# Kernel tuning notes

Measured on AMD Instinct MI355X. Metric: run time of the kernel, lower is better.

## Reference

```python
import jax, jax.numpy as jnp
import numpy as np

B, N, H = 32, 1024, 512
THR = 0.05  # peak_detection_threshold


def _l2norm(x):
    return x / jnp.linalg.norm(x, axis=-1, keepdims=True)


def setup_inputs() -> dict:
    key = jax.random.key(0)
    ks = jax.random.split(key, 6)
    def w(k, shape, fan_in):
        return jax.random.normal(k, shape, jnp.float32) / np.float32(np.sqrt(fan_in))
    return {
        "segment_rep": jax.random.normal(ks[0], (B, N, H), jnp.float32),
        "phn_mask": jnp.ones((B, N), jnp.float32),
        # SegmentSimilarityMeasure: Linear(2H->H), ReLU, Linear(H->1, no bias)
        "W1": w(ks[1], (2 * H, H), 2 * H),
        "b1": jnp.zeros((H,), jnp.float32),
        "W2": w(ks[2], (H, 1), H),
        # word_enc: Linear(H->H), ReLU, Linear(H->H)
        "We1": w(ks[3], (H, H), H),
        "be1": jnp.zeros((H,), jnp.float32),
        "We2": w(ks[4], (H, H), H),
        "be2": jnp.zeros((H,), jnp.float32),
    }


def _forward(segment_rep, phn_mask, W1, b1, W2, We1, be1, We2, be2):
    Bs, Np, Hd = segment_rep.shape
    # adjacent segment similarity: MLP on concat of l2-normalized neighbors -> (B, N-1)
    cat = jnp.concatenate([_l2norm(segment_rep[:, :-1, :]), _l2norm(segment_rep[:, 1:, :])], axis=2)
    S = (jax.nn.relu(cat @ W1 + b1) @ W2)[..., 0]

    # relative dissimilarity
    Smin = jnp.min(S, axis=1, keepdims=True)
    Smax = jnp.max(S, axis=1, keepdims=True)
    D = 1.0 - (S - Smin) / (Smax - Smin)

    # peak detector (faithful to original, incl. final overwrite of first-order cols -2:)
    z = jnp.zeros_like(D)
    fo = z
    fo = fo.at[:, 0].set(jnp.maximum(D[:, 0] - D[:, 1], 0.0))
    fo = fo.at[:, 1:-1].set(jnp.minimum(jnp.maximum(D[:, 1:-1] - D[:, :-2], 0.0),
                                        jnp.maximum(D[:, 1:-1] - D[:, 2:], 0.0)))
    fo = fo.at[:, -1].set(jnp.maximum(D[:, -1] - D[:, -2], 0.0))
    so = z
    so = so.at[:, 0:2].set(jnp.maximum(D[:, 0:2] - D[:, 2:4], 0.0))
    so = so.at[:, 2:-2].set(jnp.minimum(jnp.maximum(D[:, 2:-2] - D[:, :-4], 0.0),
                                        jnp.maximum(D[:, 2:-2] - D[:, 4:], 0.0)))
    fo = fo.at[:, -2:].set(jnp.maximum(D[:, -2:] - D[:, -4:-2], 0.0))  # replicates original code
    P = jnp.minimum(jnp.maximum(jnp.maximum(fo, so) - THR, 0.0), fo)

    # pad, mask, straight-through hard boundaries
    P = jnp.pad(P, ((0, 0), (0, 1)))
    P = jax.nn.relu(P + (phn_mask - 1.0))
    b_soft = jnp.tanh(10.0 * P)
    b_hard = jnp.tanh(100000.0 * P)
    b = b_soft + jax.lax.stop_gradient(b_hard - b_soft)
    b = jnp.cumsum(b, axis=1)  # (B, N)
    b = b + (b[:, :1] == 0).astype(b.dtype)  # per-row +1 if b[:,0]==0
    num_word_segments = b[:, -1].astype(jnp.int32) + 1  # (B,)

    # U: column j holds j+1 for j < num_word_segments[i], else -100000. Nmax = N (static bound).
    cols = jnp.arange(1, Np + 1, dtype=jnp.int32)  # (Nmax,)
    U = jnp.where(cols[None, :] <= num_word_segments[:, None],
                  cols.astype(segment_rep.dtype)[None, :], -100000.0)  # (B, Nmax)

    V = U[:, None, :] - b[:, :, None]  # (B, N, Nmax)
    Wseg = 1.0 - jnp.tanh(100000.0 * jnp.abs(V))
    Wseg = Wseg / jnp.sum(Wseg, axis=1, keepdims=True)
    Wseg = jnp.nan_to_num(Wseg)

    # pool: (B, Nmax, N) @ (B, N, H) -> (B, Nmax, H)
    word_rep = jnp.einsum('bnm,bnh->bmh', Wseg, segment_rep)
    word_masks = jnp.where(word_rep == 0, 0.0, 1.0)
    out = jax.nn.relu(word_rep @ We1 + be1) @ We2 + be2
    return out * word_masks


def reference(segment_rep, phn_mask, W1, b1, W2, We1, be1, We2, be2):
    return _forward(segment_rep, phn_mask, W1, b1, W2, We1, be1, We2, be2)
```

## Files before the change

### kernel.cpp

```cpp
#include <hip/hip_runtime.h>

#define BB 32
#define NN 1024
#define HH 512
#define NS 1023

typedef unsigned short u16;
typedef unsigned int   u32;
typedef __attribute__((ext_vector_type(8))) short bf16x8;
typedef __attribute__((ext_vector_type(4))) float f32x4;

__device__ __forceinline__ float bf2f(u16 h) {
  union { u32 u; float f; } c; c.u = ((u32)h) << 16; return c.f;
}
__device__ __forceinline__ u16 f2bf(float f) {
  union { float f; u32 u; } c; c.f = f;
  u32 u = c.u;
  return (u16)((u + 0x7fffu + ((u >> 16) & 1u)) >> 16);
}
__device__ __forceinline__ void split_bf(float x, u16& hi, u16& lo) {
  hi = f2bf(x);
  lo = f2bf(x - bf2f(hi));
}
__device__ __forceinline__ void dma16(const u16* g, u16* l) {
  __builtin_amdgcn_global_load_lds(
      (const __attribute__((address_space(1))) u32*)g,
      (__attribute__((address_space(3))) u32*)l, 16, 0, 0);
}

__global__ __launch_bounds__(64) void k_prep_a(const float* __restrict__ seg,
                                               u16* __restrict__ ahi,
                                               u16* __restrict__ alo) {
  int row = blockIdx.x, lane = threadIdx.x;
  const float4* p = (const float4*)(seg + ((size_t)row << 9) + lane * 8);
  float4 a = p[0], b = p[1];
  float v[8] = {a.x, a.y, a.z, a.w, b.x, b.y, b.z, b.w};
  float s = 0.f;
#pragma unroll
  for (int i = 0; i < 8; ++i) s += v[i] * v[i];
#pragma unroll
  for (int m = 32; m; m >>= 1) s += __shfl_xor(s, m, 64);
  float nrm = sqrtf(s);
  u16 h[8], l[8];
#pragma unroll
  for (int i = 0; i < 8; ++i) split_bf(v[i] / nrm, h[i], l[i]);
  size_t off = ((size_t)row << 9) + lane * 8;
  *(uint4*)(ahi + off) = make_uint4(h[0] | (h[1] << 16), h[2] | (h[3] << 16),
                                    h[4] | (h[5] << 16), h[6] | (h[7] << 16));
  *(uint4*)(alo + off) = make_uint4(l[0] | (l[1] << 16), l[2] | (l[3] << 16),
                                    l[4] | (l[5] << 16), l[6] | (l[7] << 16));
}

__global__ __launch_bounds__(256) void k_tr(const float* __restrict__ src,
                                            u16* __restrict__ dh,
                                            u16* __restrict__ dl,
                                            int K, int N) {
  __shared__ u16 Th[64 * 66], Tl[64 * 66];
  int nb = blockIdx.x * 64, kb = blockIdx.y * 64;
  int tid = threadIdx.x;
#pragma unroll
  for (int i = 0; i < 16; ++i) {
    int e = tid + i * 256;
    int r = e >> 6, c = e & 63;
    float v = src[(size_t)(kb + r) * N + nb + c];
    u16 hi, lo; split_bf(v, hi, lo);
    Th[c * 66 + r] = hi;
    Tl[c * 66 + r] = lo;
  }
  __syncthreads();
#pragma unroll
  for (int i = 0; i < 16; ++i) {
    int e = tid + i * 256;
    int n = e >> 6, k = e & 63;
    dh[(size_t)(nb + n) * K + kb + k] = Th[n * 66 + k];
    if (dl) dl[(size_t)(nb + n) * K + kb + k] = Tl[n * 66 + k];
  }
}

__global__ __launch_bounds__(512, 2) void k_sgemm(const u16* __restrict__ ahi,
                                                  const u16* __restrict__ alo,
                                                  const u16* __restrict__ w1h,
                                                  const u16* __restrict__ w1l,
                                                  const float* __restrict__ b1,
                                                  const float* __restrict__ W2,
                                                  float* __restrict__ Spart) {
  __shared__ u16 Ah[2][256 * 32];
  __shared__ u16 Al[2][256 * 32];
  __shared__ u16 Bh[2][256 * 32];
  __shared__ u16 Bl[2][256 * 32];

  const int tid  = threadIdx.x;
  const int wave = tid >> 6, lane = tid & 63;
  const int quad = lane >> 4, l15 = lane & 15;
  const int wm = wave >> 2, wn = wave & 3;
  const int r_in = lane >> 2, c_in = lane & 3;
  const int nblk = blockIdx.x, mblk = blockIdx.y;
  const int mrow0 = mblk * 256;
  const int ncol0 = nblk * 256;

#define SG_AH(tb_, ks_)                                                      \
  {                                                                          \
    int k0_ = (ks_) * 32, half_ = k0_ >> 9, cb_ = k0_ & 511;                 \
    int g0_ = mrow0 + wave * 32 + r_in + half_;                              \
    int g1_ = g0_ + 16;                                                      \
    if (g0_ > 32767) g0_ = 32767;                                            \
    if (g1_ > 32767) g1_ = 32767;                                            \
    dma16(ahi + ((((size_t)g0_) << 9) + cb_ + c_in * 8),                     \
          &Ah[tb_][(wave * 32) * 32]);                                       \
    dma16(ahi + ((((size_t)g1_) << 9) + cb_ + c_in * 8),                     \
          &Ah[tb_][(wave * 32 + 16) * 32]);                                  \
  }
#define SG_AL(tb_, ks_)                                                      \
  {                                                                          \
    int k0_ = (ks_) * 32, half_ = k0_ >> 9, cb_ = k0_ & 511;                 \
    int g0_ = mrow0 + wave * 32 + r_in + half_;                              \
    int g1_ = g0_ + 16;                                                      \
    if (g0_ > 32767) g0_ = 32767;                                            \
    if (g1_ > 32767) g1_ = 32767;                                            \
    dma16(alo + ((((size_t)g0_) << 9) + cb_ + c_in * 8),                     \
          &Al[tb_][(wave * 32) * 32]);                                       \
    dma16(alo + ((((size_t)g1_) << 9) + cb_ + c_in * 8),                     \
          &Al[tb_][(wave * 32 + 16) * 32]);                                  \
  }
#define SG_BH(tb_, ks_)                                                      \
  {                                                                          \
    int k0_ = (ks_) * 32;                                                    \
    int n0_ = ncol0 + wave * 32 + r_in;                                      \
    dma16(w1h + (((size_t)n0_) << 10) + k0_ + c_in * 8,                      \
          &Bh[tb_][(wave * 32) * 32]);                                       \
    dma16(w1h + (((size_t)(n0_ + 16)) << 10) + k0_ + c_in * 8,               \
          &Bh[tb_][(wave * 32 + 16) * 32]);                                  \
  }
#define SG_BL(tb_, ks_)                                                      \
  {                                                                          \
    int k0_ = (ks_) * 32;                                                    \
    int n0_ = ncol0 + wave * 32 + r_in;                                      \
    dma16(w1l + (((size_t)n0_) << 10) + k0_ + c_in * 8,                      \
          &Bl[tb_][(wave * 32) * 32]);                                       \
    dma16(w1l + (((size_t)(n0_ + 16)) << 10) + k0_ + c_in * 8,               \
          &Bl[tb_][(wave * 32 + 16) * 32]);                                  \
  }

  f32x4 acc[8][4];
#pragma unroll
  for (int mi = 0; mi < 8; ++mi)
#pragma unroll
    for (int ni = 0; ni < 4; ++ni) acc[mi][ni] = (f32x4){0.f, 0.f, 0.f, 0.f};

  SG_AH(0, 0) SG_BH(0, 0) SG_BL(0, 0) SG_AL(0, 0)
  asm volatile("s_waitcnt vmcnt(4)" ::: "memory");
  __builtin_amdgcn_s_barrier();

  for (int ks = 0; ks < 32; ++ks) {
    const int bb = ks & 1;
    const int nx = (ks + 1 < 32) ? ks + 1 : 31;
    bf16x8 ah[8], al[8], bh[4], bl[4];

#pragma unroll
    for (int mi = 0; mi < 8; ++mi)
      ah[mi] = *(const bf16x8*)&Ah[bb][(wm * 128 + mi * 16 + l15) * 32 + quad * 8];
#pragma unroll
    for (int ni = 0; ni < 4; ++ni)
      bh[ni] = *(const bf16x8*)&Bh[bb][(wn * 64 + ni * 16 + l15) * 32 + quad * 8];
    SG_AH(bb ^ 1, nx) SG_BH(bb ^ 1, nx)
    asm volatile("s_waitcnt lgkmcnt(0)" ::: "memory");
    __builtin_amdgcn_sched_barrier(0);
    __builtin_amdgcn_s_setprio(1);
#pragma unroll
    for (int ni = 0; ni < 4; ++ni)
#pragma unroll
      for (int mi = 0; mi < 8; ++mi)
        acc[mi][ni] = __builtin_amdgcn_mfma_f32_16x16x32_bf16(ah[mi], bh[ni], acc[mi][ni], 0, 0, 0);
    __builtin_amdgcn_s_setprio(0);
    asm volatile("s_waitcnt vmcnt(6)" ::: "memory");
    __builtin_amdgcn_s_barrier();

#pragma unroll
    for (int ni = 0; ni < 4; ++ni)
      bl[ni] = *(const bf16x8*)&Bl[bb][(wn * 64 + ni * 16 + l15) * 32 + quad * 8];
    SG_BL(bb ^ 1, nx) SG_AL(bb ^ 1, nx)
    asm volatile("s_waitcnt lgkmcnt(0)" ::: "memory");
    __builtin_amdgcn_sched_barrier(0);
    __builtin_amdgcn_s_setprio(1);
#pragma unroll
    for (int ni = 0; ni < 4; ++ni)
#pragma unroll
      for (int mi = 0; mi < 8; ++mi)
        acc[mi][ni] = __builtin_amdgcn_mfma_f32_16x16x32_bf16(ah[mi], bl[ni], acc[mi][ni], 0, 0, 0);
    __builtin_amdgcn_s_setprio(0);
    asm volatile("s_waitcnt vmcnt(8)" ::: "memory");
    __builtin_amdgcn_s_barrier();

#pragma unroll
    for (int mi = 0; mi < 8; ++mi)
      al[mi] = *(const bf16x8*)&Al[bb][(wm * 128 + mi * 16 + l15) * 32 + quad * 8];
    asm volatile("s_waitcnt lgkmcnt(0)" ::: "memory");
    __builtin_amdgcn_sched_barrier(0);
    __builtin_amdgcn_s_setprio(1);
#pragma unroll
    for (int ni = 0; ni < 4; ++ni)
#pragma unroll
      for (int mi = 0; mi < 8; ++mi)
        acc[mi][ni] = __builtin_amdgcn_mfma_f32_16x16x32_bf16(al[mi], bh[ni], acc[mi][ni], 0, 0, 0);
    __builtin_amdgcn_s_setprio(0);
    asm volatile("s_waitcnt vmcnt(4)" ::: "memory");
    __builtin_amdgcn_s_barrier();
  }
#undef SG_AH
#undef SG_AL
#undef SG_BH
#undef SG_BL

  asm volatile("s_waitcnt vmcnt(0)" ::: "memory");
  __syncthreads();

  float* red = (float*)&Ah[0][0];
  float b1v[4], w2v[4];
#pragma unroll
  for (int ni = 0; ni < 4; ++ni) {
    int n_g = ncol0 + wn * 64 + ni * 16 + l15;
    b1v[ni] = b1[n_g];
    w2v[ni] = W2[n_g];
  }
#pragma unroll
  for (int mi = 0; mi < 8; ++mi) {
#pragma unroll
    for (int reg = 0; reg < 4; ++reg) {
      float part = 0.f;
#pragma unroll
      for (int ni = 0; ni < 4; ++ni) {
        float h = acc[mi][ni][reg] + b1v[ni];
        h = h > 0.f ? h : 0.f;
        part = fmaf(h, w2v[ni], part);
      }
#pragma unroll
      for (int m = 8; m; m >>= 1) part += __shfl_xor(part, m, 64);
      if (l15 == 0) red[wave * 128 + mi * 16 + quad * 4 + reg] = part;
    }
  }
  __syncthreads();
  if (tid < 256) {
    int wmr = tid >> 7, rl = tid & 127;
    float s = red[(wmr * 4 + 0) * 128 + rl] + red[(wmr * 4 + 1) * 128 + rl]
            + red[(wmr * 4 + 2) * 128 + rl] + red[(wmr * 4 + 3) * 128 + rl];
    int grow = mrow0 + tid;
    int b = grow >> 10, n = grow & 1023;
    if (n < NS)
      Spart[((size_t)nblk * BB + b) * NN + n] = s;
  }
}

__global__ __launch_bounds__(256) void k_row(const float* __restrict__ S0,
                                             const float* __restrict__ S1,
                                             const float* __restrict__ mask,
                                             int* __restrict__ assign,
                                             float* __restrict__ weight,
                                             float* __restrict__ total,
                                             int* __restrict__ startn,
                                             int* __restrict__ endn) {
  int b = blockIdx.x, tid = threadIdx.x;
  __shared__ float Ssh[NS];
  __shared__ float Dsh[NS];
  __shared__ float tsh[NN];
  __shared__ float bsh[NN];
  __shared__ float totl[NN];
  __shared__ int   stl[NN];
  __shared__ int   enl[NN];
  __shared__ float red[256];

  for (int n = tid; n < NS; n += 256)
    Ssh[n] = S0[((size_t)b << 10) + n] + S1[((size_t)b << 10) + n];
  __syncthreads();

  float mn = INFINITY, mx = -INFINITY;
  for (int n = tid; n < NS; n += 256) {
    float v = Ssh[n];
    mn = fminf(mn, v); mx = fmaxf(mx, v);
  }
  red[tid] = mn; __syncthreads();
  for (int s = 128; s; s >>= 1) { if (tid < s) red[tid] = fminf(red[tid], red[tid + s]); __syncthreads(); }
  float Smin = red[0]; __syncthreads();
  red[tid] = mx; __syncthreads();
  for (int s = 128; s; s >>= 1) { if (tid < s) red[tid] = fmaxf(red[tid], red[tid + s]); __syncthreads(); }
  float Smax = red[0]; __syncthreads();

  for (int n = tid; n < NS; n += 256)
    Dsh[n] = 1.0f - (Ssh[n] - Smin) / (Smax - Smin);
  __syncthreads();

  for (int n = tid; n < NN; n += 256) {
    float P;
    if (n >= NS) {
      P = 0.f;
    } else {
      float D = Dsh[n];
      float fo, so;
      if (n == 0)            fo = fmaxf(D - Dsh[1], 0.f);
      else if (n >= NS - 2)  fo = fmaxf(D - Dsh[n - 2], 0.f);
      else                   fo = fminf(fmaxf(D - Dsh[n - 1], 0.f),
                                        fmaxf(D - Dsh[n + 1], 0.f));
      if (n <= 1)            so = fmaxf(D - Dsh[n + 2], 0.f);
      else if (n >= NS - 2)  so = 0.f;
      else                   so = fminf(fmaxf(D - Dsh[n - 2], 0.f),
                                        fmaxf(D - Dsh[n + 2], 0.f));
      P = fminf(fmaxf(fmaxf(fo, so) - 0.05f, 0.f), fo);
    }
    float m = mask[((size_t)b << 10) + n];
    P = P + (m - 1.0f);
    P = P > 0.f ? P : 0.f;
    float bs = tanhf(10.0f * P);
    float bh = tanhf(100000.0f * P);
    tsh[n] = bs + (bh - bs);
  }
  __syncthreads();

  if (tid == 0) {
    float acc = 0.f;
    for (int n = 0; n < NN; n += 8) {
      float t0 = tsh[n + 0], t1 = tsh[n + 1], t2 = tsh[n + 2], t3 = tsh[n + 3];
      float t4 = tsh[n + 4], t5 = tsh[n + 5], t6 = tsh[n + 6], t7 = tsh[n + 7];
      acc += t0; bsh[n + 0] = acc; acc += t1; bsh[n + 1] = acc;
      acc += t2; bsh[n + 2] = acc; acc += t3; bsh[n + 3] = acc;
      acc += t4; bsh[n + 4] = acc; acc += t5; bsh[n + 5] = acc;
      acc += t6; bsh[n + 6] = acc; acc += t7; bsh[n + 7] = acc;
    }
  }
  __syncthreads();

  float add1 = (bsh[0] == 0.0f) ? 1.0f : 0.0f;
  int   num  = (int)(bsh[NN - 1] + add1) + 1;

  for (int mi = tid; mi < NN; mi += 256) { totl[mi] = 0.f; stl[mi] = 1 << 30; enl[mi] = -1; }
  __syncthreads();

  for (int n = tid; n < NN; n += 256) {
    float bv = bsh[n] + add1;
    float kf = rintf(bv);
    int   k  = (int)kf;
    int   a  = -1; float w = 0.f;
    if (k >= 1 && k <= num && k <= NN) {
      float v = fabsf(kf - bv);
      w = 1.0f - tanhf(100000.0f * v);
      if (w > 0.f) {
        a = k - 1;
        atomicAdd(&totl[a], w);
        atomicMin(&stl[a], n);
        atomicMax(&enl[a], n);
      } else {
        a = -1; w = 0.f;
      }
    }
    assign[((size_t)b << 10) + n] = a;
    weight[((size_t)b << 10) + n] = w;
  }
  __syncthreads();
  for (int mi = tid; mi < NN; mi += 256) {
    total [((size_t)b << 10) + mi] = totl[mi];
    startn[((size_t)b << 10) + mi] = stl[mi];
    endn  [((size_t)b << 10) + mi] = enl[mi];
  }
}

__global__ __launch_bounds__(64) void k_pool(const float* __restrict__ seg,
                                             const int* __restrict__ assign,
                                             const float* __restrict__ weight,
                                             const float* __restrict__ total,
                                             const int* __restrict__ startn,
                                             const int* __restrict__ endn,
                                             u16* hrep,
                                             unsigned char* __restrict__ mb) {
  int bm = blockIdx.x;
  int b  = bm >> 10, m = bm & 1023;
  int lane = threadIdx.x;
  float acc[8] = {0.f, 0.f, 0.f, 0.f, 0.f, 0.f, 0.f, 0.f};
  float tm = total[bm];
  if (tm > 0.f) {
    int s = startn[bm], e = endn[bm];
    for (int n = s; n <= e; ++n) {
      if (assign[((size_t)b << 10) + n] != m) continue;
      float coef = weight[((size_t)b << 10) + n] / tm;
      const float4* p = (const float4*)(seg + (((size_t)b << 10) + n) * HH + lane * 8);
      float4 x = p[0], y = p[1];
      acc[0] = fmaf(coef, x.x, acc[0]); acc[1] = fmaf(coef, x.y, acc[1]);
      acc[2] = fmaf(coef, x.z, acc[2]); acc[3] = fmaf(coef, x.w, acc[3]);
      acc[4] = fmaf(coef, y.x, acc[4]); acc[5] = fmaf(coef, y.y, acc[5]);
      acc[6] = fmaf(coef, y.z, acc[6]); acc[7] = fmaf(coef, y.w, acc[7]);
    }
  }
  u16 h[8];
  unsigned int mbyte = 0;
#pragma unroll
  for (int j = 0; j < 8; ++j) {
    h[j] = f2bf(acc[j]);
    mbyte |= (acc[j] == 0.f ? 1u : 0u) << j;
  }
  *(uint4*)(hrep + ((size_t)bm << 10) + lane * 8) =
      make_uint4(h[0] | (h[1] << 16), h[2] | (h[3] << 16),
                 h[4] | (h[5] << 16), h[6] | (h[7] << 16));
  mb[((size_t)bm << 6) + lane] = (unsigned char)mbyte;
}

__global__ __launch_bounds__(512, 4) void k_g(const u16* asrc,
                                              const u16* __restrict__ bmat,
                                              const float* __restrict__ bias,
                                              const unsigned char* __restrict__ mb,
                                              float* outp,
                                              u16* hid,
                                              int a_off, int mode) {
  __shared__ u16 As[3][64 * 32];
  __shared__ u16 Bs[2][512 * 32];

  const int tid  = threadIdx.x;
  const int wave = tid >> 6, lane = tid & 63;
  const int quad = lane >> 4, l15 = lane & 15;
  const int wm = wave >> 2, wn = wave & 3;
  const int r_in = lane >> 2, c_in = lane & 3;
  const int mrow0 = blockIdx.x * 64;

#define SGB(tb_, ks_)                                                        \
  {                                                                          \
    int k0_ = (ks_) * 32;                                                    \
    _Pragma("unroll")                                                        \
    for (int g_ = 0; g_ < 4; ++g_) {                                         \
      int n_ = wave * 64 + g_ * 16 + r_in;                                   \
      dma16(bmat + (size_t)n_ * 512 + k0_ + c_in * 8,                        \
            &Bs[tb_][(wave * 64 + g_ * 16) * 32]);                           \
    }                                                                        \
  }
#define SGA(sl_, ks_)                                                        \
  {                                                                          \
    if (wave < 4) {                                                          \
      int k0_ = (ks_) * 32;                                                  \
      int row_ = wave * 16 + r_in;                                           \
      dma16(asrc + ((size_t)(mrow0 + row_) << 10) + a_off + k0_ + c_in * 8,  \
            &As[sl_][(wave * 16) * 32]);                                     \
    }                                                                        \
  }

  f32x4 acc[2][8];
#pragma unroll
  for (int mi = 0; mi < 2; ++mi)
#pragma unroll
    for (int ni = 0; ni < 8; ++ni) acc[mi][ni] = (f32x4){0.f, 0.f, 0.f, 0.f};

  SGB(0, 0) SGA(0, 0) SGA(1, 1)
  if (wave < 4) { asm volatile("s_waitcnt vmcnt(1)" ::: "memory"); }
  else          { asm volatile("s_waitcnt vmcnt(0)" ::: "memory"); }
  __builtin_amdgcn_s_barrier();

  for (int ks = 0; ks < 16; ++ks) {
    const int bb = ks & 1;
    const int ra = ks % 3;
    const int nb = (ks + 1 < 16) ? ks + 1 : 15;
    const int na = (ks + 2 < 16) ? ks + 2 : 15;
    SGB(bb ^ 1, nb)
    SGA((ks + 2) % 3, na)
    bf16x8 a[2], b[8];
#pragma unroll
    for (int mi = 0; mi < 2; ++mi)
      a[mi] = *(const bf16x8*)&As[ra][(wm * 32 + mi * 16 + l15) * 32 + quad * 8];
#pragma unroll
    for (int ni = 0; ni < 8; ++ni)
      b[ni] = *(const bf16x8*)&Bs[bb][(wn * 128 + ni * 16 + l15) * 32 + quad * 8];
    asm volatile("s_waitcnt lgkmcnt(0)" ::: "memory");
    __builtin_amdgcn_sched_barrier(0);
    __builtin_amdgcn_s_setprio(1);
#pragma unroll
    for (int ni = 0; ni < 8; ++ni)
#pragma unroll
      for (int mi = 0; mi < 2; ++mi)
        acc[mi][ni] = __builtin_amdgcn_mfma_f32_16x16x32_bf16(a[mi], b[ni], acc[mi][ni], 0, 0, 0);
    __builtin_amdgcn_s_setprio(0);
    if (wave < 4) { asm volatile("s_waitcnt vmcnt(1)" ::: "memory"); }
    else          { asm volatile("s_waitcnt vmcnt(0)" ::: "memory"); }
    __builtin_amdgcn_s_barrier();
  }
#undef SGB
#undef SGA
  asm volatile("s_waitcnt vmcnt(0)" ::: "memory");

  float bv[8];
#pragma unroll
  for (int ni = 0; ni < 8; ++ni) bv[ni] = bias[wn * 128 + ni * 16 + l15];

  if (mode == 1) {
#pragma unroll
    for (int mi = 0; mi < 2; ++mi)
#pragma unroll
      for (int ni = 0; ni < 8; ++ni)
#pragma unroll
        for (int reg = 0; reg < 4; ++reg) {
          int col = wn * 128 + ni * 16 + l15;
          int row = mrow0 + wm * 32 + mi * 16 + quad * 4 + reg;
          float h = acc[mi][ni][reg] + bv[ni];
          h = h > 0.f ? h : 0.f;
          hid[((size_t)row << 10) + 512 + col] = f2bf(h);
        }
  } else {
#pragma unroll
    for (int mi = 0; mi < 2; ++mi)
#pragma unroll
      for (int ni = 0; ni < 8; ++ni)
#pragma unroll
        for (int reg = 0; reg < 4; ++reg) {
          int col = wn * 128 + ni * 16 + l15;
          int row = mrow0 + wm * 32 + mi * 16 + quad * 4 + reg;
          float o = acc[mi][ni][reg] + bv[ni];
          unsigned char m8 = mb[((size_t)row << 6) + (col >> 3)];
          outp[((size_t)row << 9) + col] = ((m8 >> (col & 7)) & 1) ? 0.f : o;
        }
  }
}

__global__ void k_diag(float* __restrict__ out, int hostcode) {
  if (hostcode != 0) out[0] = (float)hostcode;
}

extern "C" void kernel_launch(void* const* d_in, const int* in_sizes, int n_in,
                              void* d_out, int out_size, void* d_ws, size_t ws_size,
                              hipStream_t stream) {
  const float* seg  = (const float*)d_in[0];
  const float* mask = (const float*)d_in[1];
  const float* W1   = (const float*)d_in[2];
  const float* b1   = (const float*)d_in[3];
  const float* W2   = (const float*)d_in[4];
  const float* We1  = (const float*)d_in[5];
  const float* be1  = (const float*)d_in[6];
  const float* We2  = (const float*)d_in[7];
  const float* be2  = (const float*)d_in[8];

  const size_t NROW = (size_t)BB * NN;
  float* ws = (float*)d_ws;
  float* S0     = ws;
  float* S1     = S0 + NROW;
  int*   assign = (int*)(S1 + NROW);
  float* weight = (float*)(assign + NROW);
  float* total  = weight + NROW;
  int*   startn = (int*)(total + NROW);
  int*   endn   = startn + NROW;
  u16*   w1h    = (u16*)(endn + NROW);
  u16*   w1l    = w1h + (size_t)512 * 1024;
  u16*   we1t   = w1l + (size_t)512 * 1024;
  u16*   we2t   = we1t + (size_t)512 * 512;

  float* out = (float*)d_out;
  u16*   ahi = (u16*)d_out;
  u16*   alo = ahi + (size_t)NROW * HH;
  u16*   hrep = (u16*)d_out;
  unsigned char* mbuf = (unsigned char*)w1h;

  int hostcode = 0;
  if (ws_size < (size_t)7 * NROW * 4 + (size_t)3 * 1024 * 1024) hostcode += 32768;
  if (out_size != 16777216) hostcode += 8192;

  k_prep_a<<<dim3(BB * NN), dim3(64), 0, stream>>>(seg, ahi, alo);
  k_tr    <<<dim3(8, 16), dim3(256), 0, stream>>>(W1, w1h, w1l, 1024, 512);
  k_tr    <<<dim3(8, 8),  dim3(256), 0, stream>>>(We1, we1t, (u16*)nullptr, 512, 512);
  k_tr    <<<dim3(8, 8),  dim3(256), 0, stream>>>(We2, we2t, (u16*)nullptr, 512, 512);
  k_sgemm <<<dim3(2, 128), dim3(512), 0, stream>>>(ahi, alo, w1h, w1l, b1, W2, S0);
  k_row   <<<dim3(BB), dim3(256), 0, stream>>>(S0, S1, mask, assign, weight, total, startn, endn);
  k_pool  <<<dim3(BB * NN), dim3(64), 0, stream>>>(seg, assign, weight, total, startn, endn, hrep, mbuf);
  k_g     <<<dim3(512), dim3(512), 0, stream>>>(hrep, we1t, be1, mbuf, out, hrep, 0,   1);
  k_g     <<<dim3(512), dim3(512), 0, stream>>>(hrep, we2t, be2, mbuf, out, hrep, 512, 2);
  k_diag  <<<dim3(1), dim3(1), 0, stream>>>(out, hostcode);
}
```

Baseline: 322.1 us.

## Merge weight transposes, remap sgemm blocks per XCD, deepen k_g A pipeline

The three weight-transpose launches become a single launch that uses blockIdx.z to pick the matrix, with excess blocks exiting early. The sgemm grid is flattened and remapped so that consecutive M tiles stay on the same XCD, aiming for better L2 reuse of the A rows. In the word-encoder GEMM, the A tiles get a 4-deep buffer with prefetch distance 3. Loads are also split by wave role: waves 0-3 fetch A and waves 4-7 fetch B. These changes cut launch overhead and aim to hide load latency, at the cost of more LDS and an uneven share of load work across waves.

```diff
diff --git a/kernel.cpp b/kernel.cpp
--- a/kernel.cpp
+++ b/kernel.cpp
@@ -51,11 +51,20 @@
                                     l[4] | (l[5] << 16), l[6] | (l[7] << 16));
 }
 
-__global__ __launch_bounds__(256) void k_tr(const float* __restrict__ src,
-                                            u16* __restrict__ dh,
-                                            u16* __restrict__ dl,
-                                            int K, int N) {
+__global__ __launch_bounds__(256) void k_tr3(const float* __restrict__ W1,
+                                             const float* __restrict__ We1,
+                                             const float* __restrict__ We2,
+                                             u16* __restrict__ w1h,
+                                             u16* __restrict__ w1l,
+                                             u16* __restrict__ we1t,
+                                             u16* __restrict__ we2t) {
   __shared__ u16 Th[64 * 66], Tl[64 * 66];
+  int z = blockIdx.z;
+  const float* src; u16 *dh, *dl; int K, N;
+  if (z == 0)      { src = W1;  dh = w1h;  dl = w1l;          K = 1024; N = 512; }
+  else if (z == 1) { src = We1; dh = we1t; dl = (u16*)0;      K = 512;  N = 512; }
+  else             { src = We2; dh = we2t; dl = (u16*)0;      K = 512;  N = 512; }
+  if (blockIdx.y * 64 >= K) return;
   int nb = blockIdx.x * 64, kb = blockIdx.y * 64;
   int tid = threadIdx.x;
 #pragma unroll
@@ -94,7 +103,10 @@
   const int quad = lane >> 4, l15 = lane & 15;
   const int wm = wave >> 2, wn = wave & 3;
   const int r_in = lane >> 2, c_in = lane & 3;
-  const int nblk = blockIdx.x, mblk = blockIdx.y;
+  const int w    = blockIdx.x;
+  const int xcd  = w & 7, slot = w >> 3;
+  const int nblk = slot & 1;
+  const int mblk = xcd * 16 + (slot >> 1);
   const int mrow0 = mblk * 256;
   const int ncol0 = nblk * 256;
 
@@ -407,7 +419,7 @@
                                               float* outp,
                                               u16* hid,
                                               int a_off, int mode) {
-  __shared__ u16 As[3][64 * 32];
+  __shared__ u16 As[4][64 * 32];
   __shared__ u16 Bs[2][512 * 32];
 
   const int tid  = threadIdx.x;
@@ -418,23 +430,21 @@
   const int mrow0 = blockIdx.x * 64;
 
 #define SGB(tb_, ks_)                                                        \
-  {                                                                          \
+  if (wave >= 4) {                                                           \
     int k0_ = (ks_) * 32;                                                    \
     _Pragma("unroll")                                                        \
-    for (int g_ = 0; g_ < 4; ++g_) {                                         \
-      int n_ = wave * 64 + g_ * 16 + r_in;                                   \
+    for (int g_ = 0; g_ < 8; ++g_) {                                         \
+      int n_ = (wave - 4) * 128 + g_ * 16 + r_in;                            \
       dma16(bmat + (size_t)n_ * 512 + k0_ + c_in * 8,                        \
-            &Bs[tb_][(wave * 64 + g_ * 16) * 32]);                           \
+            &Bs[tb_][((wave - 4) * 128 + g_ * 16) * 32]);                    \
     }                                                                        \
   }
 #define SGA(sl_, ks_)                                                        \
-  {                                                                          \
-    if (wave < 4) {                                                          \
-      int k0_ = (ks_) * 32;                                                  \
-      int row_ = wave * 16 + r_in;                                           \
-      dma16(asrc + ((size_t)(mrow0 + row_) << 10) + a_off + k0_ + c_in * 8,  \
-            &As[sl_][(wave * 16) * 32]);                                     \
-    }                                                                        \
+  if (wave < 4) {                                                            \
+    int k0_ = (ks_) * 32;                                                    \
+    int row_ = wave * 16 + r_in;                                             \
+    dma16(asrc + ((size_t)(mrow0 + row_) << 10) + a_off + k0_ + c_in * 8,    \
+          &As[sl_][(wave * 16) * 32]);                                       \
   }
 
   f32x4 acc[2][8];
@@ -443,18 +453,18 @@
 #pragma unroll
     for (int ni = 0; ni < 8; ++ni) acc[mi][ni] = (f32x4){0.f, 0.f, 0.f, 0.f};
 
-  SGB(0, 0) SGA(0, 0) SGA(1, 1)
-  if (wave < 4) { asm volatile("s_waitcnt vmcnt(1)" ::: "memory"); }
+  SGB(0, 0) SGA(0, 0) SGA(1, 1) SGA(2, 2)
+  if (wave < 4) { asm volatile("s_waitcnt vmcnt(2)" ::: "memory"); }
   else          { asm volatile("s_waitcnt vmcnt(0)" ::: "memory"); }
   __builtin_amdgcn_s_barrier();
 
   for (int ks = 0; ks < 16; ++ks) {
     const int bb = ks & 1;
-    const int ra = ks % 3;
+    const int ra = ks & 3;
     const int nb = (ks + 1 < 16) ? ks + 1 : 15;
-    const int na = (ks + 2 < 16) ? ks + 2 : 15;
+    const int na = (ks + 3 < 16) ? ks + 3 : 15;
     SGB(bb ^ 1, nb)
-    SGA((ks + 2) % 3, na)
+    SGA((ks + 3) & 3, na)
     bf16x8 a[2], b[8];
 #pragma unroll
     for (int mi = 0; mi < 2; ++mi)
@@ -471,7 +481,7 @@
       for (int mi = 0; mi < 2; ++mi)
         acc[mi][ni] = __builtin_amdgcn_mfma_f32_16x16x32_bf16(a[mi], b[ni], acc[mi][ni], 0, 0, 0);
     __builtin_amdgcn_s_setprio(0);
-    if (wave < 4) { asm volatile("s_waitcnt vmcnt(1)" ::: "memory"); }
+    if (wave < 4) { asm volatile("s_waitcnt vmcnt(2)" ::: "memory"); }
     else          { asm volatile("s_waitcnt vmcnt(0)" ::: "memory"); }
     __builtin_amdgcn_s_barrier();
   }
@@ -554,10 +564,8 @@
   if (out_size != 16777216) hostcode += 8192;
 
   k_prep_a<<<dim3(BB * NN), dim3(64), 0, stream>>>(seg, ahi, alo);
-  k_tr    <<<dim3(8, 16), dim3(256), 0, stream>>>(W1, w1h, w1l, 1024, 512);
-  k_tr    <<<dim3(8, 8),  dim3(256), 0, stream>>>(We1, we1t, (u16*)nullptr, 512, 512);
-  k_tr    <<<dim3(8, 8),  dim3(256), 0, stream>>>(We2, we2t, (u16*)nullptr, 512, 512);
-  k_sgemm <<<dim3(2, 128), dim3(512), 0, stream>>>(ahi, alo, w1h, w1l, b1, W2, S0);
+  k_tr3   <<<dim3(8, 16, 3), dim3(256), 0, stream>>>(W1, We1, We2, w1h, w1l, we1t, we2t);
+  k_sgemm <<<dim3(256), dim3(512), 0, stream>>>(ahi, alo, w1h, w1l, b1, W2, S0);
   k_row   <<<dim3(BB), dim3(256), 0, stream>>>(S0, S1, mask, assign, weight, total, startn, endn);
   k_pool  <<<dim3(BB * NN), dim3(64), 0, stream>>>(seg, assign, weight, total, startn, endn, hrep, mbuf);
   k_g     <<<dim3(512), dim3(512), 0, stream>>>(hrep, we1t, be1, mbuf, out, hrep, 0,   1);
```

Measured after the change: 331.6 us. +3.0%, slower.

## Merge weight transposes, remap GEMM blocks per XCD, simplify pipeline sync

Applied to the files above, without the earlier changes.

Fuses the three weight-transpose launches into one 3D launch and packs four rows per block in the normalize kernel, so there are fewer launches and fewer tiny blocks. The similarity GEMM grid is remapped so that blocks on the same XCD share A row tiles, which should improve L2 reuse. Its main loop now issues all four next-stage DMA loads up front and uses a single __syncthreads per K-step in place of the hand-tuned vmcnt waits and three barriers. This changes how global loads overlap with the MFMA phases and leaves the LDS-read-versus-MFMA ordering to the compiler.

```diff
diff --git a/kernel.cpp b/kernel.cpp
--- a/kernel.cpp
+++ b/kernel.cpp
@@ -28,10 +28,11 @@
       (__attribute__((address_space(3))) u32*)l, 16, 0, 0);
 }
 
-__global__ __launch_bounds__(64) void k_prep_a(const float* __restrict__ seg,
-                                               u16* __restrict__ ahi,
-                                               u16* __restrict__ alo) {
-  int row = blockIdx.x, lane = threadIdx.x;
+__global__ __launch_bounds__(256) void k_prep_a(const float* __restrict__ seg,
+                                                u16* __restrict__ ahi,
+                                                u16* __restrict__ alo) {
+  int row = blockIdx.x * 4 + (threadIdx.x >> 6);
+  int lane = threadIdx.x & 63;
   const float4* p = (const float4*)(seg + ((size_t)row << 9) + lane * 8);
   float4 a = p[0], b = p[1];
   float v[8] = {a.x, a.y, a.z, a.w, b.x, b.y, b.z, b.w};
@@ -51,11 +52,20 @@
                                     l[4] | (l[5] << 16), l[6] | (l[7] << 16));
 }
 
-__global__ __launch_bounds__(256) void k_tr(const float* __restrict__ src,
-                                            u16* __restrict__ dh,
-                                            u16* __restrict__ dl,
-                                            int K, int N) {
+__global__ __launch_bounds__(256) void k_tr3(const float* __restrict__ W1,
+                                             const float* __restrict__ We1,
+                                             const float* __restrict__ We2,
+                                             u16* __restrict__ w1h,
+                                             u16* __restrict__ w1l,
+                                             u16* __restrict__ we1t,
+                                             u16* __restrict__ we2t) {
   __shared__ u16 Th[64 * 66], Tl[64 * 66];
+  int z = blockIdx.z;
+  const float* src; u16 *dh, *dl; int K, N;
+  if (z == 0)      { src = W1;  dh = w1h;  dl = w1l;          K = 1024; N = 512; }
+  else if (z == 1) { src = We1; dh = we1t; dl = (u16*)0;      K = 512;  N = 512; }
+  else             { src = We2; dh = we2t; dl = (u16*)0;      K = 512;  N = 512; }
+  if (blockIdx.y * 64 >= K) return;
   int nb = blockIdx.x * 64, kb = blockIdx.y * 64;
   int tid = threadIdx.x;
 #pragma unroll
@@ -94,7 +104,10 @@
   const int quad = lane >> 4, l15 = lane & 15;
   const int wm = wave >> 2, wn = wave & 3;
   const int r_in = lane >> 2, c_in = lane & 3;
-  const int nblk = blockIdx.x, mblk = blockIdx.y;
+  const int w    = blockIdx.x;
+  const int xcd  = w & 7, slot = w >> 3;
+  const int nblk = slot & 1;
+  const int mblk = xcd * 16 + (slot >> 1);
   const int mrow0 = mblk * 256;
   const int ncol0 = nblk * 256;
 
@@ -148,71 +161,51 @@
     for (int ni = 0; ni < 4; ++ni) acc[mi][ni] = (f32x4){0.f, 0.f, 0.f, 0.f};
 
   SG_AH(0, 0) SG_BH(0, 0) SG_BL(0, 0) SG_AL(0, 0)
-  asm volatile("s_waitcnt vmcnt(4)" ::: "memory");
-  __builtin_amdgcn_s_barrier();
+  __syncthreads();
 
   for (int ks = 0; ks < 32; ++ks) {
     const int bb = ks & 1;
     const int nx = (ks + 1 < 32) ? ks + 1 : 31;
+
+    SG_AH(bb ^ 1, nx) SG_BH(bb ^ 1, nx) SG_BL(bb ^ 1, nx) SG_AL(bb ^ 1, nx)
+
     bf16x8 ah[8], al[8], bh[4], bl[4];
-
 #pragma unroll
     for (int mi = 0; mi < 8; ++mi)
       ah[mi] = *(const bf16x8*)&Ah[bb][(wm * 128 + mi * 16 + l15) * 32 + quad * 8];
 #pragma unroll
     for (int ni = 0; ni < 4; ++ni)
       bh[ni] = *(const bf16x8*)&Bh[bb][(wn * 64 + ni * 16 + l15) * 32 + quad * 8];
-    SG_AH(bb ^ 1, nx) SG_BH(bb ^ 1, nx)
-    asm volatile("s_waitcnt lgkmcnt(0)" ::: "memory");
-    __builtin_amdgcn_sched_barrier(0);
     __builtin_amdgcn_s_setprio(1);
 #pragma unroll
     for (int ni = 0; ni < 4; ++ni)
 #pragma unroll
       for (int mi = 0; mi < 8; ++mi)
         acc[mi][ni] = __builtin_amdgcn_mfma_f32_16x16x32_bf16(ah[mi], bh[ni], acc[mi][ni], 0, 0, 0);
-    __builtin_amdgcn_s_setprio(0);
-    asm volatile("s_waitcnt vmcnt(6)" ::: "memory");
-    __builtin_amdgcn_s_barrier();
-
 #pragma unroll
     for (int ni = 0; ni < 4; ++ni)
       bl[ni] = *(const bf16x8*)&Bl[bb][(wn * 64 + ni * 16 + l15) * 32 + quad * 8];
-    SG_BL(bb ^ 1, nx) SG_AL(bb ^ 1, nx)
-    asm volatile("s_waitcnt lgkmcnt(0)" ::: "memory");
-    __builtin_amdgcn_sched_barrier(0);
-    __builtin_amdgcn_s_setprio(1);
 #pragma unroll
     for (int ni = 0; ni < 4; ++ni)
 #pragma unroll
       for (int mi = 0; mi < 8; ++mi)
         acc[mi][ni] = __builtin_amdgcn_mfma_f32_16x16x32_bf16(ah[mi], bl[ni], acc[mi][ni], 0, 0, 0);
-    __builtin_amdgcn_s_setprio(0);
-    asm volatile("s_waitcnt vmcnt(8)" ::: "memory");
-    __builtin_amdgcn_s_barrier();
-
 #pragma unroll
     for (int mi = 0; mi < 8; ++mi)
       al[mi] = *(const bf16x8*)&Al[bb][(wm * 128 + mi * 16 + l15) * 32 + quad * 8];
-    asm volatile("s_waitcnt lgkmcnt(0)" ::: "memory");
-    __builtin_amdgcn_sched_barrier(0);
-    __builtin_amdgcn_s_setprio(1);
 #pragma unroll
     for (int ni = 0; ni < 4; ++ni)
 #pragma unroll
       for (int mi = 0; mi < 8; ++mi)
         acc[mi][ni] = __builtin_amdgcn_mfma_f32_16x16x32_bf16(al[mi], bh[ni], acc[mi][ni], 0, 0, 0);
     __builtin_amdgcn_s_setprio(0);
-    asm volatile("s_waitcnt vmcnt(4)" ::: "memory");
-    __builtin_amdgcn_s_barrier();
+
+    __syncthreads();
   }
 #undef SG_AH
 #undef SG_AL
 #undef SG_BH
 #undef SG_BL
-
-  asm volatile("s_waitcnt vmcnt(0)" ::: "memory");
-  __syncthreads();
 
   float* red = (float*)&Ah[0][0];
   float b1v[4], w2v[4];
@@ -553,11 +546,9 @@
   if (ws_size < (size_t)7 * NROW * 4 + (size_t)3 * 1024 * 1024) hostcode += 32768;
   if (out_size != 16777216) hostcode += 8192;
 
-  k_prep_a<<<dim3(BB * NN), dim3(64), 0, stream>>>(seg, ahi, alo);
-  k_tr    <<<dim3(8, 16), dim3(256), 0, stream>>>(W1, w1h, w1l, 1024, 512);
-  k_tr    <<<dim3(8, 8),  dim3(256), 0, stream>>>(We1, we1t, (u16*)nullptr, 512, 512);
-  k_tr    <<<dim3(8, 8),  dim3(256), 0, stream>>>(We2, we2t, (u16*)nullptr, 512, 512);
-  k_sgemm <<<dim3(2, 128), dim3(512), 0, stream>>>(ahi, alo, w1h, w1l, b1, W2, S0);
+  k_prep_a<<<dim3(BB * NN / 4), dim3(256), 0, stream>>>(seg, ahi, alo);
+  k_tr3   <<<dim3(8, 16, 3), dim3(256), 0, stream>>>(W1, We1, We2, w1h, w1l, we1t, we2t);
+  k_sgemm <<<dim3(256), dim3(512), 0, stream>>>(ahi, alo, w1h, w1l, b1, W2, S0);
   k_row   <<<dim3(BB), dim3(256), 0, stream>>>(S0, S1, mask, assign, weight, total, startn, endn);
   k_pool  <<<dim3(BB * NN), dim3(64), 0, stream>>>(seg, assign, weight, total, startn, endn, hrep, mbuf);
   k_g     <<<dim3(512), dim3(512), 0, stream>>>(hrep, we1t, be1, mbuf, out, hrep, 0,   1);
```

Result: no change. 319.4 us (-0.9%).
